# Kernel tuning notes

Hardware: AMD Instinct MI355X
Metric: run time of the kernel (lower is better)

Reference implementation:

```python
import jax, jax.numpy as jnp
import numpy as np

N_HEADS = 16
MASK_NEG = -1e32


def setup_inputs() -> dict:
    key = jax.random.key(0)
    k0, k1, k2, k3, k4 = jax.random.split(key, 5)
    B, S, D = 8, 1024, 1024
    return {
        "q": jax.random.normal(k0, (B, S, D), dtype=jnp.float32),
        "k": jax.random.normal(k1, (B, S, D), dtype=jnp.float32),
        "v1": jax.random.normal(k2, (B, S, D), dtype=jnp.float32),
        "v2": jax.random.normal(k3, (B, S, D), dtype=jnp.float32),
        "counter_attention_mask": jax.random.randint(k4, (B, S), 0, 2, dtype=jnp.int32),
    }


def reference(q, k, v1, v2, counter_attention_mask):
    B, S, D = q.shape
    H = N_HEADS
    dk = D // H

    def split_heads(x):
        return x.reshape(B, S, H, dk).transpose(0, 2, 1, 3)  # [B,H,S,dk]

    qh, kh, v1h, v2h = split_heads(q), split_heads(k), split_heads(v1), split_heads(v2)

    # scaled dot-product scores [B,H,S,S]
    scores = jnp.einsum("bhqd,bhkd->bhqk", qh, kh) / jnp.sqrt(jnp.float32(dk))

    # create_mask(input, 0): allowed only where key_idx < query_idx (strict causal)
    i = jnp.arange(S)[:, None]
    j = jnp.arange(S)[None, :]
    allowed = j < i  # [S,S]
    scores = jnp.where(allowed[None, None], scores, MASK_NEG)

    # first softmax
    p = jax.nn.softmax(scores, axis=-1)

    # counter-attention mask: zero out masked key columns (per batch, all heads/rows)
    cm = counter_attention_mask[:, None, None, :]  # [B,1,1,S]
    p = jnp.where(cm == 1, jnp.float32(0.0), p)

    # second softmax over the (partially zeroed) probabilities
    p = jax.nn.softmax(p, axis=-1)

    # zero the first query row (pad_zero concat in the original)
    p = p.at[:, :, 0, :].set(0.0)

    out1 = jnp.einsum("bhqk,bhkd->bhqd", p, v1h)
    out2 = jnp.einsum("bhqk,bhkd->bhqd", p, v2h)

    def merge_heads(x):
        return x.transpose(0, 2, 1, 3).reshape(B, S, D)

    return merge_heads(out1), merge_heads(out2)
```

## Files before the change

kernel.cpp:

```cpp
#include <hip/hip_runtime.h>
#include <hip/hip_bf16.h>

#define B_ 8
#define S_ 1024
#define D_ 1024
#define H_ 16
#define DK_ 64
#define BH_ (B_ * H_)
#define NQ 8
#define QTASK 256
#define NPERS 768

typedef float f32x4 __attribute__((ext_vector_type(4)));
typedef short s16x8 __attribute__((ext_vector_type(8)));
typedef short s16x4 __attribute__((ext_vector_type(4)));

#define EXP2F(x) __builtin_amdgcn_exp2f(x)
#define LOG2E 1.44269504088896f

static __device__ __forceinline__ short f2b(float f) {
  unsigned u = __builtin_bit_cast(unsigned, f);
  u = u + 0x7FFFu + ((u >> 16) & 1u);
  return (short)(u >> 16);
}
static __device__ __forceinline__ short f2bn(float f) {
  __hip_bfloat16 h = __float2bfloat16(f);
  return __builtin_bit_cast(short, h);
}

static __device__ __forceinline__ int slotf(int g, int e) {
  return (e < 4) ? (4 * g + e) : (16 + 4 * g + (e - 4));
}


__global__ __launch_bounds__(256) void prep_k(const float* __restrict__ k,
                                              short* __restrict__ kb) {
  const int bid = blockIdx.x;
  const int s0 = (bid & 63) * 16;
  const int b = bid >> 6;
  const int tid = threadIdx.x;
#pragma unroll
  for (int it = 0; it < 8; ++it) {
    int li = it * 256 + tid;
    int s = s0 + (li >> 7);
    int ch = li & 127;
    int h = ch >> 3;
    int dk0 = (ch & 7) * 8;
    const float* src = k + ((size_t)(b * S_ + s)) * D_ + ch * 8;
    s16x8 o;
#pragma unroll
    for (int e = 0; e < 8; ++e) o[e] = f2b(src[e]);
    *(s16x8*)(kb + ((size_t)((b * H_ + h) * S_ + s)) * DK_ + dk0) = o;
  }
}

__global__ __launch_bounds__(256) void prep_v(const float* __restrict__ v1,
                                              const float* __restrict__ v2,
                                              const int* __restrict__ cm,
                                              short* __restrict__ v1f,
                                              short* __restrict__ v2f,
                                              float* __restrict__ vs) {
  const int bid = blockIdx.x;
  const int sg = bid & 3;
  const int h = (bid >> 2) & 15;
  const int b = bid >> 6;
  const int tid = threadIdx.x;
  const int db = tid >> 6;
  const int lane = tid & 63;
  const int r = lane & 15;
  const int g = lane >> 4;
  const size_t inbase = (size_t)b * S_ * D_ + h * DK_ + db * 16 + r;
  const int* cmb = cm + b * S_;
  float s1 = 0.f, s2 = 0.f;
#pragma unroll
  for (int it = 0; it < 8; ++it) {
    int jt = sg * 8 + it;
    int j0 = jt * 32;
    s16x8 o1, o2;
#pragma unroll
    for (int e = 0; e < 8; ++e) {
      int j = j0 + slotf(g, e);
      float a = v1[inbase + (size_t)j * D_];
      float c = v2[inbase + (size_t)j * D_];
      s1 += a;
      s2 += c;
      bool msk = (cmb[j] == 1);
      o1[e] = msk ? (short)0 : f2b(a);
      o2[e] = msk ? (short)0 : f2b(c);
    }
    size_t off = (((size_t)((b * H_ + h) * 32 + jt) * 4 + db) * 64 + lane) * 8;
    *(s16x8*)(v1f + off) = o1;
    *(s16x8*)(v2f + off) = o2;
  }
  s1 += __shfl_xor(s1, 16);
  s1 += __shfl_xor(s1, 32);
  s2 += __shfl_xor(s2, 16);
  s2 += __shfl_xor(s2, 32);
  if (g == 0) {
    int dd = db * 16 + r;
    atomicAdd(&vs[(size_t)b * D_ + h * DK_ + dd], s1);
    atomicAdd(&vs[(size_t)(B_ + b) * D_ + h * DK_ + dd], s2);
  }
}

__global__ __launch_bounds__(256, 3) void attn_series2s(
    const float* __restrict__ q, const short* __restrict__ kb,
    const short* __restrict__ v1f, const short* __restrict__ v2f,
    const int* __restrict__ cm, const float* __restrict__ vs,
    unsigned* __restrict__ counters, float* __restrict__ out) {
  const int tid = threadIdx.x;
  const int wid = tid >> 6;
  const int lane = tid & 63;
  const int r = lane & 15;
  const int g = lane >> 4;

  unsigned xcc = 0;
  asm volatile("s_getreg_b32 %0, hwreg(HW_REG_XCC_ID)" : "=s"(xcc));
  const int xq = (int)(xcc & 7u);

  __shared__ __align__(16) char sbuf[2][12288];
  __shared__ unsigned cmw[32];
  __shared__ int taskS;

  const int srow = tid >> 3;
  const int sch = tid & 7;

#define SLK(reg, jtv) reg = *(const s16x8*)(kbh + (size_t)(jtv)*2048 + tid * 8);
#define SLV(d1, d2, jtv)                                           \
  {                                                                \
    d1 = *(const s16x8*)(v1bh + (size_t)(jtv)*2048 + tid * 8);     \
    d2 = *(const s16x8*)(v2bh + (size_t)(jtv)*2048 + tid * 8);     \
  }
#define SWK(buf, reg) \
  *(s16x8*)((buf) + srow * 128 + ((sch ^ (srow & 7)) * 16)) = reg;
#define SWV(buf, d1, d2)                        \
  {                                             \
    *(s16x8*)((buf) + 4096 + tid * 16) = d1;    \
    *(s16x8*)((buf) + 8192 + tid * 16) = d2;    \
  }
#define KFRAG(sK, row, quad) \
  (*(const s16x8*)((sK) + (row)*128 + (((quad) ^ ((row)&7)) * 16)))

  s16x8 ones;
#pragma unroll
  for (int e = 0; e < 8; ++e) ones[e] = (short)0x3F80;

  float* out1 = out;
  float* out2 = out + (size_t)B_ * S_ * D_;

  for (int qi = 0; qi < NQ; ++qi) {
    const int qq = (xq + qi) & 7;
    for (;;) {
      __syncthreads();
      if (tid == 0) taskS = (int)atomicAdd(&counters[qq * 64], 1u);
      __syncthreads();
      const int task = taskS;
      if (task >= QTASK) break;

      const int seg = 15 - (task >> 4);
      const int bh = (task & 15) * 8 + qq;
      const int b = bh >> 4, h = bh & 15;

      const int qw = seg * 64 + wid * 16;
      const int iq = qw + r;
      const int njt = 2 * seg + 2;

      {
        const int* cmb = cm + b * S_;
#pragma unroll
        for (int it = 0; it < 4; ++it) {
          unsigned long long m = __ballot(cmb[it * 256 + tid] == 1);
          if (lane == 0) {
            int w0 = it * 8 + wid * 2;
            cmw[w0] = (unsigned)m;
            cmw[w0 + 1] = (unsigned)(m >> 32);
          }
        }
      }

      const float qscale = 0.125f * LOG2E;
      s16x8 qf0, qf1;
      {
        const float* qp = q + ((size_t)(b * S_ + qw + r)) * D_ + h * DK_;
#pragma unroll
        for (int e = 0; e < 8; ++e) qf0[e] = f2bn(qp[8 * g + e] * qscale);
#pragma unroll
        for (int e = 0; e < 8; ++e) qf1[e] = f2bn(qp[32 + 8 * g + e] * qscale);
      }

      const short* kbh = kb + (size_t)bh * S_ * DK_;
      const short* v1bh = v1f + (size_t)bh * 32 * 2048;
      const short* v2bh = v2f + (size_t)bh * 32 * 2048;

      f32x4 a11[4], a12[4], a21[4], a22[4];
#pragma unroll
      for (int d0 = 0; d0 < 4; ++d0) {
        a11[d0] = (f32x4){0.f, 0.f, 0.f, 0.f};
        a12[d0] = (f32x4){0.f, 0.f, 0.f, 0.f};
        a21[d0] = (f32x4){0.f, 0.f, 0.f, 0.f};
        a22[d0] = (f32x4){0.f, 0.f, 0.f, 0.f};
      }
      f32x4 za = {0.f, 0.f, 0.f, 0.f};
      f32x4 t1a = {0.f, 0.f, 0.f, 0.f};
      f32x4 t2a = {0.f, 0.f, 0.f, 0.f};

      {
        s16x8 rk, rv1, rv2;
        SLK(rk, 0);
        SLV(rv1, rv2, 0);
        SWK(sbuf[0], rk);
        SWV(sbuf[0], rv1, rv2);
        __syncthreads();
        for (int jt = 0; jt < njt; ++jt) {
          const int jb = jt * 32;
          const char* sB = sbuf[jt & 1];
          const bool pf = (jt + 1 < njt);
          s16x8 rk2, rv12, rv22;
          if (pf) {
            SLK(rk2, jt + 1);
            SLV(rv12, rv22, jt + 1);
          }
          if (jb < qw + 16) {
            s16x8 k00 = KFRAG(sB, r, g);
            s16x8 k01 = KFRAG(sB, r, 4 + g);
            s16x8 k10 = KFRAG(sB, 16 + r, g);
            s16x8 k11 = KFRAG(sB, 16 + r, 4 + g);
            f32x4 s0 = {0.f, 0.f, 0.f, 0.f}, s1 = {0.f, 0.f, 0.f, 0.f};
            s0 = __builtin_amdgcn_mfma_f32_16x16x32_bf16(k00, qf0, s0, 0, 0, 0);
            s0 = __builtin_amdgcn_mfma_f32_16x16x32_bf16(k01, qf1, s0, 0, 0, 0);
            s1 = __builtin_amdgcn_mfma_f32_16x16x32_bf16(k10, qf0, s1, 0, 0, 0);
            s1 = __builtin_amdgcn_mfma_f32_16x16x32_bf16(k11, qf1, s1, 0, 0, 0);
            const unsigned cw = cmw[jt];
            const bool cb = (jb + 32 > qw);
            float w1[8], w2[8];
#pragma unroll
            for (int s2 = 0; s2 < 2; ++s2) {
              f32x4 sv = s2 ? s1 : s0;
#pragma unroll
              for (int e = 0; e < 4; ++e) {
                float pe = EXP2F(sv[e]);
                if (cb) {
                  int j = jb + s2 * 16 + 4 * g + e;
                  pe = (j < iq) ? pe : 0.f;
                }
                int o = s2 * 4 + e;
                w1[o] = pe;
                w2[o] = pe * pe;
              }
            }
            s16x8 wa1, wa2, mf;
#pragma unroll
            for (int o = 0; o < 8; ++o) {
              wa1[o] = f2bn(w1[o]);
              wa2[o] = f2bn(w2[o]);
              int kk = slotf(g, o);
              mf[o] = ((cw >> kk) & 1u) ? (short)0 : (short)0x3F80;
            }
            s16x8 vb1[4], vb2[4];
#pragma unroll
            for (int db = 0; db < 4; ++db) {
              vb1[db] = *(const s16x8*)(sB + 4096 + (db * 64 + lane) * 16);
              vb2[db] = *(const s16x8*)(sB + 8192 + (db * 64 + lane) * 16);
            }
#pragma unroll
            for (int db = 0; db < 4; ++db) {
              a11[db] = __builtin_amdgcn_mfma_f32_16x16x32_bf16(wa1, vb1[db], a11[db], 0, 0, 0);
              a21[db] = __builtin_amdgcn_mfma_f32_16x16x32_bf16(wa1, vb2[db], a21[db], 0, 0, 0);
              a12[db] = __builtin_amdgcn_mfma_f32_16x16x32_bf16(wa2, vb1[db], a12[db], 0, 0, 0);
              a22[db] = __builtin_amdgcn_mfma_f32_16x16x32_bf16(wa2, vb2[db], a22[db], 0, 0, 0);
            }
            za = __builtin_amdgcn_mfma_f32_16x16x32_bf16(wa1, ones, za, 0, 0, 0);
            t1a = __builtin_amdgcn_mfma_f32_16x16x32_bf16(wa1, mf, t1a, 0, 0, 0);
            t2a = __builtin_amdgcn_mfma_f32_16x16x32_bf16(wa2, mf, t2a, 0, 0, 0);
          }
          if (pf) {
            SWK(sbuf[(jt + 1) & 1], rk2);
            SWV(sbuf[(jt + 1) & 1], rv12, rv22);
          }
          __syncthreads();
        }
      }

      const float* vs1 = vs + (size_t)b * D_ + h * DK_;
      const float* vs2 = vs + (size_t)(B_ + b) * D_ + h * DK_;

#pragma unroll
      for (int e = 0; e < 4; ++e) {
        const float iz = (za[e] > 0.f) ? (1.f / za[e]) : 0.f;
        const float f1 = iz;
        const float f2v = 0.5f * iz * iz;
        const float Z2 = (float)S_ + t1a[e] * f1 + t2a[e] * f2v;
        const float izz = 1.f / Z2;
        const float gg1 = f1 * izz;
        const float gg2 = f2v * izz;
        const float ggc = izz;
        int io = qw + 4 * g + e;
        bool zero = (io == 0);
        size_t ro = ((size_t)(b * S_) + io) * D_ + h * DK_;
#pragma unroll
        for (int db = 0; db < 4; ++db) {
          int dd = db * 16 + r;
          float o1 = a11[db][e] * gg1 + a12[db][e] * gg2 + vs1[dd] * ggc;
          float o2 = a21[db][e] * gg1 + a22[db][e] * gg2 + vs2[dd] * ggc;
          out1[ro + dd] = zero ? 0.f : o1;
          out2[ro + dd] = zero ? 0.f : o2;
        }
      }
    }
  }
#undef SLK
#undef SLV
#undef SWK
#undef SWV
#undef KFRAG
}


__global__ __launch_bounds__(256) void vsum_kernel(const float* __restrict__ v1,
                                                   const float* __restrict__ v2,
                                                   float* __restrict__ vs) {
  int bid = blockIdx.x;
  int sc = bid & 7, dc = (bid >> 3) & 3, b = bid >> 5;
  int d = dc * 256 + threadIdx.x;
  const float* p1 = v1 + ((size_t)b * S_ + sc * 128) * D_ + d;
  const float* p2 = v2 + ((size_t)b * S_ + sc * 128) * D_ + d;
  float s1 = 0.f, s2 = 0.f;
  for (int j = 0; j < 128; ++j) {
    s1 += p1[(size_t)j * D_];
    s2 += p2[(size_t)j * D_];
  }
  atomicAdd(&vs[b * D_ + d], s1);
  atomicAdd(&vs[B_ * D_ + b * D_ + d], s2);
}

__global__ __launch_bounds__(256) void dualattn_fallback(
    const float* __restrict__ q, const float* __restrict__ k,
    const float* __restrict__ v1, const float* __restrict__ v2,
    const int* __restrict__ cm, const float* __restrict__ vs,
    float* __restrict__ out) {
  const int bid = blockIdx.x;
  const int qt = bid & 15;
  const int h = (bid >> 4) & 15;
  const int b = bid >> 8;
  const int tid = threadIdx.x;
  const int wid = tid >> 6;
  const int lane = tid & 63;
  const int r = lane & 15;
  const int g = lane >> 4;
  const int qw = qt * 64 + wid * 16;
  const int iq = qw + r;

  __shared__ __align__(16) char kbuf[32 * 128];
  __shared__ __align__(16) char vtb1[64 * 64];
  __shared__ __align__(16) char vtb2[64 * 64];
  __shared__ unsigned cmw[32];

  {
    const int* cmb = cm + b * S_;
#pragma unroll
    for (int it = 0; it < 4; ++it) {
      int c = cmb[it * 256 + tid];
      unsigned long long m = __ballot(c == 1);
      if (lane == 0) {
        int w0 = (it * 256 + wid * 64) >> 5;
        cmw[w0] = (unsigned)m;
        cmw[w0 + 1] = (unsigned)(m >> 32);
      }
    }
  }

  s16x8 qf0, qf1;
  {
    const float* qp = q + ((size_t)(b * S_) + qw + r) * D_ + h * DK_;
#pragma unroll
    for (int e = 0; e < 8; ++e) qf0[e] = f2b(qp[8 * g + e] * 0.125f);
#pragma unroll
    for (int e = 0; e < 8; ++e) qf1[e] = f2b(qp[32 + 8 * g + e] * 0.125f);
  }

  const int njt = 2 * qt + 2;
  const float* kbase = k + (size_t)(b * S_) * D_ + h * DK_;
  const float* v1base = v1 + (size_t)(b * S_) * D_ + h * DK_;
  const float* v2base = v2 + (size_t)(b * S_) * D_ + h * DK_;
  const int srow = tid >> 3;
  const int sch = tid & 7;

  float m1 = -INFINITY, Z1 = 0.f;
  for (int jt = 0; jt < njt; ++jt) {
    const int jbase = jt * 32;
    __syncthreads();
    {
      const float* kr = kbase + (size_t)(jbase + srow) * D_ + sch * 8;
      s16x8 pk;
#pragma unroll
      for (int e = 0; e < 8; ++e) pk[e] = f2b(kr[e]);
      *(s16x8*)(kbuf + srow * 128 + ((sch ^ (srow & 7)) * 16)) = pk;
    }
    __syncthreads();
    if (jbase < qw + 16) {
#pragma unroll
      for (int sub = 0; sub < 2; ++sub) {
        const int jsb = jbase + sub * 16;
        if (jsb < qw + 16) {
          const int row = sub * 16 + r;
          s16x8 ka0 = *(const s16x8*)(kbuf + row * 128 + ((g ^ (row & 7)) * 16));
          s16x8 ka1 = *(const s16x8*)(kbuf + row * 128 + (((4 + g) ^ (row & 7)) * 16));
          f32x4 sv = {0.f, 0.f, 0.f, 0.f};
          sv = __builtin_amdgcn_mfma_f32_16x16x32_bf16(ka0, qf0, sv, 0, 0, 0);
          sv = __builtin_amdgcn_mfma_f32_16x16x32_bf16(ka1, qf1, sv, 0, 0, 0);
          float tm = m1;
#pragma unroll
          for (int e = 0; e < 4; ++e) {
            int j = jsb + 4 * g + e;
            if (j < iq) tm = fmaxf(tm, sv[e]);
          }
          if (tm > m1) { Z1 *= __expf(m1 - tm); m1 = tm; }
#pragma unroll
          for (int e = 0; e < 4; ++e) {
            int j = jsb + 4 * g + e;
            if (j < iq) Z1 += __expf(sv[e] - tm);
          }
        }
      }
    }
  }
#pragma unroll
  for (int off = 16; off < 64; off <<= 1) {
    float mo = __shfl_xor(m1, off);
    float zo = __shfl_xor(Z1, off);
    float mn = fmaxf(m1, mo);
    if (mn > -INFINITY) {
      Z1 = Z1 * __expf(m1 - mn) + zo * __expf(mo - mn);
      m1 = mn;
    }
  }
  float z1i;
  if (m1 > -INFINITY) { z1i = 1.f / Z1; }
  else { z1i = 0.f; m1 = 0.f; }

  f32x4 acc1[4], acc2[4];
#pragma unroll
  for (int d0 = 0; d0 < 4; ++d0) {
    acc1[d0] = (f32x4){0.f, 0.f, 0.f, 0.f};
    acc2[d0] = (f32x4){0.f, 0.f, 0.f, 0.f};
  }
  float wsum = 0.f;

  for (int jt = 0; jt < njt; ++jt) {
    const int jbase = jt * 32;
    __syncthreads();
    {
      const float* kr = kbase + (size_t)(jbase + srow) * D_ + sch * 8;
      s16x8 pk;
#pragma unroll
      for (int e = 0; e < 8; ++e) pk[e] = f2b(kr[e]);
      *(s16x8*)(kbuf + srow * 128 + ((sch ^ (srow & 7)) * 16)) = pk;
      const float* v1r = v1base + (size_t)(jbase + srow) * D_ + sch * 8;
      const float* v2r = v2base + (size_t)(jbase + srow) * D_ + sch * 8;
#pragma unroll
      for (int e = 0; e < 8; ++e) {
        int dd = sch * 8 + e;
        int off = dd * 64 + (((srow >> 2) ^ (dd & 7)) * 8) + (srow & 3) * 2;
        *(short*)(vtb1 + off) = f2b(v1r[e]);
        *(short*)(vtb2 + off) = f2b(v2r[e]);
      }
    }
    __syncthreads();
    if (jbase < qw + 16) {
      const unsigned cmword = cmw[jbase >> 5];
      float w[8];
#pragma unroll
      for (int sub = 0; sub < 2; ++sub) {
        const int jsb = jbase + sub * 16;
        if (jsb < qw + 16) {
          const int row = sub * 16 + r;
          s16x8 ka0 = *(const s16x8*)(kbuf + row * 128 + ((g ^ (row & 7)) * 16));
          s16x8 ka1 = *(const s16x8*)(kbuf + row * 128 + (((4 + g) ^ (row & 7)) * 16));
          f32x4 sv = {0.f, 0.f, 0.f, 0.f};
          sv = __builtin_amdgcn_mfma_f32_16x16x32_bf16(ka0, qf0, sv, 0, 0, 0);
          sv = __builtin_amdgcn_mfma_f32_16x16x32_bf16(ka1, qf1, sv, 0, 0, 0);
#pragma unroll
          for (int e = 0; e < 4; ++e) {
            int j = jsb + 4 * g + e;
            float x = 0.f;
            if (j < iq && !((cmword >> (j & 31)) & 1u)) {
              float p = __expf(sv[e] - m1) * z1i;
              x = __expf(p) - 1.f;
            }
            w[sub * 4 + e] = x;
            wsum += x;
          }
        } else {
#pragma unroll
          for (int e = 0; e < 4; ++e) w[sub * 4 + e] = 0.f;
        }
      }
      s16x8 wa;
#pragma unroll
      for (int e = 0; e < 8; ++e) wa[e] = f2b(w[e]);
#pragma unroll
      for (int db = 0; db < 4; ++db) {
        const int dd = db * 16 + r;
        const int off0 = dd * 64 + ((g ^ (dd & 7)) * 8);
        const int off1 = dd * 64 + (((4 + g) ^ (dd & 7)) * 8);
        s16x4 lo1 = *(const s16x4*)(vtb1 + off0);
        s16x4 hi1 = *(const s16x4*)(vtb1 + off1);
        s16x8 vb1 = __builtin_shufflevector(lo1, hi1, 0, 1, 2, 3, 4, 5, 6, 7);
        acc1[db] = __builtin_amdgcn_mfma_f32_16x16x32_bf16(wa, vb1, acc1[db], 0, 0, 0);
        s16x4 lo2 = *(const s16x4*)(vtb2 + off0);
        s16x4 hi2 = *(const s16x4*)(vtb2 + off1);
        s16x8 vb2 = __builtin_shufflevector(lo2, hi2, 0, 1, 2, 3, 4, 5, 6, 7);
        acc2[db] = __builtin_amdgcn_mfma_f32_16x16x32_bf16(wa, vb2, acc2[db], 0, 0, 0);
      }
    }
  }

  wsum += __shfl_xor(wsum, 16);
  wsum += __shfl_xor(wsum, 32);
  const float z2 = (float)S_ + wsum;

  float* out1 = out;
  float* out2 = out + (size_t)B_ * S_ * D_;
#pragma unroll
  for (int e = 0; e < 4; ++e) {
    float z2e = __shfl(z2, 4 * g + e);
    float inv = 1.f / z2e;
    int io = qw + 4 * g + e;
    bool zero = (io == 0);
    size_t ro = ((size_t)(b * S_) + io) * D_ + h * DK_;
#pragma unroll
    for (int db = 0; db < 4; ++db) {
      int dd = db * 16 + r;
      float c1 = vs[(size_t)b * D_ + h * DK_ + dd];
      float c2 = vs[(size_t)(B_ + b) * D_ + h * DK_ + dd];
      out1[ro + dd] = zero ? 0.f : (acc1[db][e] + c1) * inv;
      out2[ro + dd] = zero ? 0.f : (acc2[db][e] + c2) * inv;
    }
  }
}


extern "C" void kernel_launch(void* const* d_in, const int* in_sizes, int n_in,
                              void* d_out, int out_size, void* d_ws, size_t ws_size,
                              hipStream_t stream) {
  (void)in_sizes; (void)n_in; (void)out_size;
  const float* q = (const float*)d_in[0];
  const float* k = (const float*)d_in[1];
  const float* v1 = (const float*)d_in[2];
  const float* v2 = (const float*)d_in[3];
  const int* cm = (const int*)d_in[4];
  float* outp = (float*)d_out;

  const size_t VS_BYTES = 2 * B_ * D_ * sizeof(float);
  const size_t CTR_BYTES = NQ * 64 * sizeof(unsigned);
  const size_t FRAG_SHORTS = (size_t)BH_ * S_ * DK_;
  const size_t FRAG_BYTES = FRAG_SHORTS * 2;
  const size_t NEED = VS_BYTES + CTR_BYTES + 3 * FRAG_BYTES;

  float* vs = (float*)d_ws;
  (void)hipMemsetAsync(d_ws, 0, VS_BYTES + CTR_BYTES, stream);

  if (ws_size >= NEED) {
    unsigned* counters = (unsigned*)((char*)d_ws + VS_BYTES);
    short* kb = (short*)((char*)d_ws + VS_BYTES + CTR_BYTES);
    short* v1f = kb + FRAG_SHORTS;
    short* v2f = v1f + FRAG_SHORTS;
    prep_k<<<B_ * (S_ / 16), 256, 0, stream>>>(k, kb);
    prep_v<<<B_ * H_ * 4, 256, 0, stream>>>(v1, v2, cm, v1f, v2f, vs);
    attn_series2s<<<NPERS, 256, 0, stream>>>(q, kb, v1f, v2f, cm, vs, counters,
                                             outp);
  } else {
    vsum_kernel<<<256, 256, 0, stream>>>(v1, v2, vs);
    dualattn_fallback<<<B_ * H_ * 16, 256, 0, stream>>>(q, k, v1, v2, cm, vs, outp);
  }
}
```

Before: 102.0 us.

## Merge prep kernels and precompute mask MFMA fragments in workspace

Combines the K and V preparation kernels into one launch, split by block index, and adds an extra block that builds a per-batch bf16 mask fragment array (0 or 1.0 in MFMA slot order) from the counter-attention mask. The attention kernel now loads this fragment directly per key tile instead of ballot-packing the mask into shared memory for every task and decoding bits per lane. This saves one kernel launch and removes the per-task mask setup and bit-decoding ALU work. In exchange each tile does an extra small global load, and a single block builds the whole mask array.

```diff
diff --git a/kernel.cpp b/kernel.cpp
--- a/kernel.cpp
+++ b/kernel.cpp
@@ -32,81 +32,89 @@
   return (e < 4) ? (4 * g + e) : (16 + 4 * g + (e - 4));
 }
 
-
-__global__ __launch_bounds__(256) void prep_k(const float* __restrict__ k,
-                                              short* __restrict__ kb) {
+__global__ __launch_bounds__(256) void prep_all(
+    const float* __restrict__ k, const float* __restrict__ v1,
+    const float* __restrict__ v2, const int* __restrict__ cm,
+    short* __restrict__ kb, short* __restrict__ v1f, short* __restrict__ v2f,
+    float* __restrict__ vs, short* __restrict__ mfrag) {
   const int bid = blockIdx.x;
-  const int s0 = (bid & 63) * 16;
-  const int b = bid >> 6;
   const int tid = threadIdx.x;
-#pragma unroll
-  for (int it = 0; it < 8; ++it) {
-    int li = it * 256 + tid;
-    int s = s0 + (li >> 7);
-    int ch = li & 127;
-    int h = ch >> 3;
-    int dk0 = (ch & 7) * 8;
-    const float* src = k + ((size_t)(b * S_ + s)) * D_ + ch * 8;
-    s16x8 o;
-#pragma unroll
-    for (int e = 0; e < 8; ++e) o[e] = f2b(src[e]);
-    *(s16x8*)(kb + ((size_t)((b * H_ + h) * S_ + s)) * DK_ + dk0) = o;
-  }
-}
-
-__global__ __launch_bounds__(256) void prep_v(const float* __restrict__ v1,
-                                              const float* __restrict__ v2,
-                                              const int* __restrict__ cm,
-                                              short* __restrict__ v1f,
-                                              short* __restrict__ v2f,
-                                              float* __restrict__ vs) {
-  const int bid = blockIdx.x;
-  const int sg = bid & 3;
-  const int h = (bid >> 2) & 15;
-  const int b = bid >> 6;
-  const int tid = threadIdx.x;
-  const int db = tid >> 6;
-  const int lane = tid & 63;
-  const int r = lane & 15;
-  const int g = lane >> 4;
-  const size_t inbase = (size_t)b * S_ * D_ + h * DK_ + db * 16 + r;
-  const int* cmb = cm + b * S_;
-  float s1 = 0.f, s2 = 0.f;
-#pragma unroll
-  for (int it = 0; it < 8; ++it) {
-    int jt = sg * 8 + it;
-    int j0 = jt * 32;
-    s16x8 o1, o2;
-#pragma unroll
-    for (int e = 0; e < 8; ++e) {
-      int j = j0 + slotf(g, e);
-      float a = v1[inbase + (size_t)j * D_];
-      float c = v2[inbase + (size_t)j * D_];
-      s1 += a;
-      s2 += c;
-      bool msk = (cmb[j] == 1);
-      o1[e] = msk ? (short)0 : f2b(a);
-      o2[e] = msk ? (short)0 : f2b(c);
-    }
-    size_t off = (((size_t)((b * H_ + h) * 32 + jt) * 4 + db) * 64 + lane) * 8;
-    *(s16x8*)(v1f + off) = o1;
-    *(s16x8*)(v2f + off) = o2;
-  }
-  s1 += __shfl_xor(s1, 16);
-  s1 += __shfl_xor(s1, 32);
-  s2 += __shfl_xor(s2, 16);
-  s2 += __shfl_xor(s2, 32);
-  if (g == 0) {
-    int dd = db * 16 + r;
-    atomicAdd(&vs[(size_t)b * D_ + h * DK_ + dd], s1);
-    atomicAdd(&vs[(size_t)(B_ + b) * D_ + h * DK_ + dd], s2);
-  }
-}
-
-__global__ __launch_bounds__(256, 3) void attn_series2s(
+
+  if (bid < 512) {
+    const int s0 = (bid & 63) * 16;
+    const int b = bid >> 6;
+#pragma unroll
+    for (int it = 0; it < 8; ++it) {
+      int li = it * 256 + tid;
+      int s = s0 + (li >> 7);
+      int ch = li & 127;
+      int h = ch >> 3;
+      int dk0 = (ch & 7) * 8;
+      const float* src = k + ((size_t)(b * S_ + s)) * D_ + ch * 8;
+      s16x8 o;
+#pragma unroll
+      for (int e = 0; e < 8; ++e) o[e] = f2b(src[e]);
+      *(s16x8*)(kb + ((size_t)((b * H_ + h) * S_ + s)) * DK_ + dk0) = o;
+    }
+  } else if (bid < 1024) {
+    const int b2 = bid - 512;
+    const int sg = b2 & 3;
+    const int h = (b2 >> 2) & 15;
+    const int b = b2 >> 6;
+    const int db = tid >> 6;
+    const int lane = tid & 63;
+    const int r = lane & 15;
+    const int g = lane >> 4;
+    const size_t inbase = (size_t)b * S_ * D_ + h * DK_ + db * 16 + r;
+    const int* cmb = cm + b * S_;
+    float s1 = 0.f, s2 = 0.f;
+#pragma unroll
+    for (int it = 0; it < 8; ++it) {
+      int jt = sg * 8 + it;
+      int j0 = jt * 32;
+      s16x8 o1, o2;
+#pragma unroll
+      for (int e = 0; e < 8; ++e) {
+        int j = j0 + slotf(g, e);
+        float a = v1[inbase + (size_t)j * D_];
+        float c = v2[inbase + (size_t)j * D_];
+        s1 += a;
+        s2 += c;
+        bool msk = (cmb[j] == 1);
+        o1[e] = msk ? (short)0 : f2b(a);
+        o2[e] = msk ? (short)0 : f2b(c);
+      }
+      size_t off = (((size_t)((b * H_ + h) * 32 + jt) * 4 + db) * 64 + lane) * 8;
+      *(s16x8*)(v1f + off) = o1;
+      *(s16x8*)(v2f + off) = o2;
+    }
+    s1 += __shfl_xor(s1, 16);
+    s1 += __shfl_xor(s1, 32);
+    s2 += __shfl_xor(s2, 16);
+    s2 += __shfl_xor(s2, 32);
+    if (g == 0) {
+      int dd = db * 16 + r;
+      atomicAdd(&vs[(size_t)b * D_ + h * DK_ + dd], s1);
+      atomicAdd(&vs[(size_t)(B_ + b) * D_ + h * DK_ + dd], s2);
+    }
+  } else {
+#pragma unroll
+    for (int i = 0; i < 32; ++i) {
+      int idx = tid * 32 + i;
+      int o = idx & 7;
+      int g = (idx >> 3) & 3;
+      int jt = (idx >> 5) & 31;
+      int b = idx >> 10;
+      int j = jt * 32 + slotf(g, o);
+      mfrag[idx] = (cm[b * S_ + j] == 1) ? (short)0 : (short)0x3F80;
+    }
+  }
+}
+
+__global__ __launch_bounds__(256, 3) void attn_series2t(
     const float* __restrict__ q, const short* __restrict__ kb,
     const short* __restrict__ v1f, const short* __restrict__ v2f,
-    const int* __restrict__ cm, const float* __restrict__ vs,
+    const short* __restrict__ mfrag, const float* __restrict__ vs,
     unsigned* __restrict__ counters, float* __restrict__ out) {
   const int tid = threadIdx.x;
   const int wid = tid >> 6;
@@ -119,7 +127,6 @@
   const int xq = (int)(xcc & 7u);
 
   __shared__ __align__(16) char sbuf[2][12288];
-  __shared__ unsigned cmw[32];
   __shared__ int taskS;
 
   const int srow = tid >> 3;
@@ -165,19 +172,6 @@
       const int iq = qw + r;
       const int njt = 2 * seg + 2;
 
-      {
-        const int* cmb = cm + b * S_;
-#pragma unroll
-        for (int it = 0; it < 4; ++it) {
-          unsigned long long m = __ballot(cmb[it * 256 + tid] == 1);
-          if (lane == 0) {
-            int w0 = it * 8 + wid * 2;
-            cmw[w0] = (unsigned)m;
-            cmw[w0 + 1] = (unsigned)(m >> 32);
-          }
-        }
-      }
-
       const float qscale = 0.125f * LOG2E;
       s16x8 qf0, qf1;
       {
@@ -191,6 +185,7 @@
       const short* kbh = kb + (size_t)bh * S_ * DK_;
       const short* v1bh = v1f + (size_t)bh * 32 * 2048;
       const short* v2bh = v2f + (size_t)bh * 32 * 2048;
+      const short* mfb = mfrag + ((size_t)b * 32 * 4 + g) * 8;
 
       f32x4 a11[4], a12[4], a21[4], a22[4];
 #pragma unroll
@@ -221,6 +216,7 @@
             SLV(rv12, rv22, jt + 1);
           }
           if (jb < qw + 16) {
+            s16x8 mf = *(const s16x8*)(mfb + (size_t)jt * 32);
             s16x8 k00 = KFRAG(sB, r, g);
             s16x8 k01 = KFRAG(sB, r, 4 + g);
             s16x8 k10 = KFRAG(sB, 16 + r, g);
@@ -230,7 +226,6 @@
             s0 = __builtin_amdgcn_mfma_f32_16x16x32_bf16(k01, qf1, s0, 0, 0, 0);
             s1 = __builtin_amdgcn_mfma_f32_16x16x32_bf16(k10, qf0, s1, 0, 0, 0);
             s1 = __builtin_amdgcn_mfma_f32_16x16x32_bf16(k11, qf1, s1, 0, 0, 0);
-            const unsigned cw = cmw[jt];
             const bool cb = (jb + 32 > qw);
             float w1[8], w2[8];
 #pragma unroll
@@ -248,13 +243,11 @@
                 w2[o] = pe * pe;
               }
             }
-            s16x8 wa1, wa2, mf;
+            s16x8 wa1, wa2;
 #pragma unroll
             for (int o = 0; o < 8; ++o) {
               wa1[o] = f2bn(w1[o]);
               wa2[o] = f2bn(w2[o]);
-              int kk = slotf(g, o);
-              mf[o] = ((cw >> kk) & 1u) ? (short)0 : (short)0x3F80;
             }
             s16x8 vb1[4], vb2[4];
 #pragma unroll
@@ -553,22 +546,23 @@
 
   const size_t VS_BYTES = 2 * B_ * D_ * sizeof(float);
   const size_t CTR_BYTES = NQ * 64 * sizeof(unsigned);
+  const size_t MF_BYTES = 8192 * sizeof(short);
   const size_t FRAG_SHORTS = (size_t)BH_ * S_ * DK_;
   const size_t FRAG_BYTES = FRAG_SHORTS * 2;
-  const size_t NEED = VS_BYTES + CTR_BYTES + 3 * FRAG_BYTES;
+  const size_t NEED = VS_BYTES + CTR_BYTES + MF_BYTES + 3 * FRAG_BYTES;
 
   float* vs = (float*)d_ws;
   (void)hipMemsetAsync(d_ws, 0, VS_BYTES + CTR_BYTES, stream);
 
   if (ws_size >= NEED) {
     unsigned* counters = (unsigned*)((char*)d_ws + VS_BYTES);
-    short* kb = (short*)((char*)d_ws + VS_BYTES + CTR_BYTES);
+    short* mfrag = (short*)((char*)d_ws + VS_BYTES + CTR_BYTES);
+    short* kb = (short*)((char*)d_ws + VS_BYTES + CTR_BYTES + MF_BYTES);
     short* v1f = kb + FRAG_SHORTS;
     short* v2f = v1f + FRAG_SHORTS;
-    prep_k<<<B_ * (S_ / 16), 256, 0, stream>>>(k, kb);
-    prep_v<<<B_ * H_ * 4, 256, 0, stream>>>(v1, v2, cm, v1f, v2f, vs);
-    attn_series2s<<<NPERS, 256, 0, stream>>>(q, kb, v1f, v2f, cm, vs, counters,
-                                             outp);
+    prep_all<<<1025, 256, 0, stream>>>(k, v1, v2, cm, kb, v1f, v2f, vs, mfrag);
+    attn_series2t<<<NPERS, 256, 0, stream>>>(q, kb, v1f, v2f, mfrag, vs,
+                                             counters, outp);
   } else {
     vsum_kernel<<<256, 256, 0, stream>>>(v1, v2, vs);
     dualattn_fallback<<<B_ * H_ * 16, 256, 0, stream>>>(q, k, v1, v2, cm, vs, outp);
```

New measurement: 98.61 us (median of 2 runs). 1.03x faster.
